# Performance work log

Measured on AMD Instinct MI355X. Metric: run time of the kernel, lower is better.

The kernel has to match this reference:

```python
import jax, jax.numpy as jnp
import numpy as np

B = 256        # number of graphs (mol rows)
N = 262144     # total residues
H = 128        # hidden_dim


def setup_inputs() -> dict:
    key = jax.random.key(0)
    ks = jax.random.split(key, 8)
    mol = jax.random.normal(ks[0], (B, H), dtype=jnp.float32)
    prot = jax.random.normal(ks[1], (N, H), dtype=jnp.float32)
    batch = jnp.sort(jax.random.randint(ks[2], (N,), 0, B)).astype(jnp.int64)
    s = 1.0 / np.sqrt(H)
    Wq = jax.random.uniform(ks[3], (H, H), jnp.float32, -s, s)
    bq = jax.random.uniform(ks[4], (H,), jnp.float32, -s, s)
    Wk = jax.random.uniform(ks[5], (H, H), jnp.float32, -s, s)
    bk = jax.random.uniform(ks[6], (H,), jnp.float32, -s, s)
    sm = 1.0 / np.sqrt(2 * H)
    Wm = jax.random.uniform(ks[7], (1, 2 * H), jnp.float32, -sm, sm)  # merge, no bias
    return {"mol": mol, "prot": prot, "batch": batch,
            "Wq": Wq, "bq": bq, "Wk": Wk, "bk": bk, "Wm": Wm}


def reference(mol, prot, batch, Wq, bq, Wk, bk, Wm):
    q = jax.nn.relu(mol @ Wq.T + bq)                      # [B, H]
    # repeat_interleave(q, degree(batch)) with sorted batch == gather q[batch]
    r = q[batch]                                          # [N, H]
    k = jax.nn.relu(prot @ Wk.T + bk)                     # [N, H]
    score = jnp.concatenate([k, r], axis=-1) @ Wm.T       # [N, 1]
    # segment softmax over residues of each graph (stable)
    m = jax.ops.segment_max(score, batch, num_segments=B)  # [B, 1]
    e = jnp.exp(score - m[batch])                          # [N, 1]
    denom = jax.ops.segment_sum(e, batch, num_segments=B)  # [B, 1]
    attn = e / denom[batch]                                # [N, 1]
    o = jax.ops.segment_sum(k * attn, batch, num_segments=B)  # [B, H]
    return (o, q)
```

## Files before the change

kernel.cpp:

```cpp
#include <hip/hip_runtime.h>
#include <hip/hip_bf16.h>

#define H      128
#define NB     256
#define NRES   262144
#define CHUNK  128
#define NCHUNK (NRES / CHUNK)
#define PIECES 64
#define REC    136

typedef __attribute__((ext_vector_type(4))) float f32x4;
typedef __attribute__((ext_vector_type(8))) short short8;

__device__ __forceinline__ short bf16cvt(float f) {
  unsigned u = __builtin_bit_cast(unsigned, f);
  unsigned r = (u + 0x7fffu + ((u >> 16) & 1u)) >> 16;
  return (short)r;
}

__device__ __forceinline__ float bf16tof(unsigned short u) {
  unsigned v = ((unsigned)u) << 16;
  return __builtin_bit_cast(float, v);
}

__device__ __forceinline__ short8 pack_bf16x8(f32x4 x, f32x4 y) {
  short8 v;
  v[0] = bf16cvt(x[0]); v[1] = bf16cvt(x[1]);
  v[2] = bf16cvt(x[2]); v[3] = bf16cvt(x[3]);
  v[4] = bf16cvt(y[0]); v[5] = bf16cvt(y[1]);
  v[6] = bf16cvt(y[2]); v[7] = bf16cvt(y[3]);
  return v;
}

__device__ __forceinline__ int lower_bound_i(const int* __restrict__ a, int n, int v) {
  int lo = 0, hi = n;
  while (lo < hi) { int mid = (lo + hi) >> 1; if (a[mid] < v) lo = mid + 1; else hi = mid; }
  return lo;
}

__global__ __launch_bounds__(256) void prep(
    const float* __restrict__ mol, const float* __restrict__ Wq,
    const float* __restrict__ bq, const float* __restrict__ Wk,
    float* __restrict__ out, short* __restrict__ wkp) {
  int bid = blockIdx.x, tid = threadIdx.x;
  if (bid < NB) {
    if (tid < H) {
      const float* mrow = mol + bid * H;
      const float* wrow = Wq + tid * H;
      float acc = bq[tid];
#pragma unroll 8
      for (int j = 0; j < H; ++j) acc = fmaf(mrow[j], wrow[j], acc);
      out[NB * H + bid * H + tid] = fmaxf(acc, 0.f);
    }
  } else {
    int slot = (bid - NB) * 256 + tid;
    int f = slot >> 6, l = slot & 63;
    int ct = f >> 2, kk = f & 3;
    const float* src = Wk + (ct * 16 + (l & 15)) * H + kk * 32 + (l >> 4) * 8;
    f32x4 x = *(const f32x4*)src;
    f32x4 y = *(const f32x4*)(src + 4);
    *(short8*)&wkp[slot * 8] = pack_bf16x8(x, y);
  }
}

__global__ __launch_bounds__(256) void chunkkern(
    const float* __restrict__ prot, const int* __restrict__ batch,
    const short* __restrict__ wkp, const float* __restrict__ bk,
    const float* __restrict__ Wm, float* __restrict__ part) {
  __shared__ short bfrag[2048 * 8];
  __shared__ unsigned short k_sh[CHUNK * 132];
  __shared__ float score_sh[CHUNK];
  __shared__ float e_sh[CHUNK];
  __shared__ float vhalf[H];
  __shared__ int   batch_sh[CHUNK];
  __shared__ float red[4], red2[4];

  int tid = threadIdx.x;
  int c0row = blockIdx.x * CHUNK;

  for (int i = tid; i < 2048; i += 256)
    *(short8*)&bfrag[i * 8] = *(const short8*)&wkp[i * 8];
  if (tid < CHUNK) batch_sh[tid] = batch[c0row + tid];
  __syncthreads();

  int w = tid >> 6, l = tid & 63;
  int cg = l & 15, kg = l >> 4;
  float wm1v[8], bkv[8];
#pragma unroll
  for (int ct = 0; ct < 8; ++ct) { wm1v[ct] = Wm[ct * 16 + cg]; bkv[ct] = bk[ct * 16 + cg]; }

#pragma unroll
  for (int tile = 0; tile < 2; ++tile) {
    int rbase = w * 32 + tile * 16;
    const float* pbase = prot + (c0row + rbase + cg) * H + kg * 8;
    short8 a[4];
#pragma unroll
    for (int kk = 0; kk < 4; ++kk) {
      f32x4 x = *(const f32x4*)(pbase + kk * 32);
      f32x4 y = *(const f32x4*)(pbase + kk * 32 + 4);
      a[kk] = pack_bf16x8(x, y);
    }
    f32x4 acc[8];
#pragma unroll
    for (int ct = 0; ct < 8; ++ct) acc[ct] = (f32x4){0.f, 0.f, 0.f, 0.f};
#pragma unroll
    for (int ct = 0; ct < 8; ++ct)
#pragma unroll
      for (int kk = 0; kk < 4; ++kk) {
        short8 bf = *(const short8*)&bfrag[((ct * 4 + kk) * 64 + l) * 8];
        acc[ct] = __builtin_amdgcn_mfma_f32_16x16x32_bf16(a[kk], bf, acc[ct], 0, 0, 0);
      }
    float p0 = 0.f, p1 = 0.f, p2 = 0.f, p3 = 0.f;
    int row0 = rbase + kg * 4;
#pragma unroll
    for (int ct = 0; ct < 8; ++ct) {
      float v0 = fmaxf(acc[ct][0] + bkv[ct], 0.f);
      float v1 = fmaxf(acc[ct][1] + bkv[ct], 0.f);
      float v2 = fmaxf(acc[ct][2] + bkv[ct], 0.f);
      float v3 = fmaxf(acc[ct][3] + bkv[ct], 0.f);
      p0 += v0 * wm1v[ct]; p1 += v1 * wm1v[ct];
      p2 += v2 * wm1v[ct]; p3 += v3 * wm1v[ct];
      int colb = ct * 16 + cg;
      k_sh[(row0 + 0) * 132 + colb] = (unsigned short)bf16cvt(v0);
      k_sh[(row0 + 1) * 132 + colb] = (unsigned short)bf16cvt(v1);
      k_sh[(row0 + 2) * 132 + colb] = (unsigned short)bf16cvt(v2);
      k_sh[(row0 + 3) * 132 + colb] = (unsigned short)bf16cvt(v3);
    }
#pragma unroll
    for (int off = 1; off < 16; off <<= 1) {
      p0 += __shfl_xor(p0, off); p1 += __shfl_xor(p1, off);
      p2 += __shfl_xor(p2, off); p3 += __shfl_xor(p3, off);
    }
    if (cg < 4) {
      int j = l & 3;
      float pv = (j == 0) ? p0 : (j == 1) ? p1 : (j == 2) ? p2 : p3;
      score_sh[rbase + kg * 4 + j] = pv;
    }
  }
  __syncthreads();

  int b0 = batch_sh[0], b1 = batch_sh[CHUNK - 1];
  int slot = blockIdx.x & (PIECES - 1);
  for (int b = b0; b <= b1; ++b) {
    int lo, hi;
    { int L = 0, R = CHUNK; while (L < R) { int M = (L + R) >> 1; if (batch_sh[M] < b) L = M + 1; else R = M; } lo = L; }
    { int L = 0, R = CHUNK; while (L < R) { int M = (L + R) >> 1; if (batch_sh[M] <= b) L = M + 1; else R = M; } hi = L; }
    if (hi > lo) {
      float x = (tid < CHUNK && tid >= lo && tid < hi) ? score_sh[tid] : -3.0e38f;
#pragma unroll
      for (int off = 32; off >= 1; off >>= 1) x = fmaxf(x, __shfl_xor(x, off));
      if (l == 0) red[w] = x;
      __syncthreads();
      float m_loc = fmaxf(fmaxf(red[0], red[1]), fmaxf(red[2], red[3]));
      float e = 0.f;
      if (tid < CHUNK && tid >= lo && tid < hi) { e = __expf(score_sh[tid] - m_loc); e_sh[tid] = e; }
      float s = e;
#pragma unroll
      for (int off = 32; off >= 1; off >>= 1) s += __shfl_xor(s, off);
      if (l == 0) red2[w] = s;
      __syncthreads();
      float s_loc = red2[0] + red2[1] + red2[2] + red2[3];
      int c = tid & 127, half = tid >> 7;
      float acc = 0.f;
      for (int r = lo + half; r < hi; r += 2)
        acc += e_sh[r] * bf16tof(k_sh[r * 132 + c]);
      if (half) vhalf[c] = acc;
      __syncthreads();
      float* pp = part + ((size_t)b * PIECES + slot) * REC;
      if (!half) pp[8 + c] = acc + vhalf[c];
      if (tid == 0) { pp[0] = m_loc; pp[1] = s_loc; }
      __syncthreads();
    }
  }
}

__global__ __launch_bounds__(128) void combine(
    const int* __restrict__ batch, const float* __restrict__ part,
    float* __restrict__ out) {
  int b = blockIdx.x, c = threadIdx.x;
  int start = lower_bound_i(batch, NRES, b);
  int end = lower_bound_i(batch, NRES, b + 1);
  if (end <= start) { out[b * H + c] = 0.f; return; }
  int c0 = start >> 7, c1 = (end - 1) >> 7;
  float m = -3.0e38f;
  for (int ch = c0; ch <= c1; ++ch)
    m = fmaxf(m, part[((size_t)b * PIECES + (ch & (PIECES - 1))) * REC]);
  float denom = 0.f, v = 0.f;
  for (int ch = c0; ch <= c1; ++ch) {
    const float* pp = part + ((size_t)b * PIECES + (ch & (PIECES - 1))) * REC;
    float wgt = __expf(pp[0] - m);
    denom += pp[1] * wgt;
    v += pp[8 + c] * wgt;
  }
  out[b * H + c] = (denom > 0.f) ? v / denom : 0.f;
}

extern "C" void kernel_launch(void* const* d_in, const int* in_sizes, int n_in,
                              void* d_out, int out_size, void* d_ws, size_t ws_size,
                              hipStream_t stream) {
  const float* mol   = (const float*)d_in[0];
  const float* prot  = (const float*)d_in[1];
  const int*   batch = (const int*)d_in[2];
  const float* Wq    = (const float*)d_in[3];
  const float* bq    = (const float*)d_in[4];
  const float* Wk    = (const float*)d_in[5];
  const float* bk    = (const float*)d_in[6];
  const float* Wm    = (const float*)d_in[7];
  float* out = (float*)d_out;

  short* wkp  = (short*)d_ws;
  float* part = (float*)((char*)d_ws + 32768);

  hipLaunchKernelGGL(prep, dim3(NB + 8), dim3(256), 0, stream, mol, Wq, bq, Wk, out, wkp);
  hipLaunchKernelGGL(chunkkern, dim3(NCHUNK), dim3(256), 0, stream, prot, batch, wkp, bk, Wm, part);
  hipLaunchKernelGGL(combine, dim3(NB), dim3(128), 0, stream, batch, part, out);
}
```

Measured before the change: 242.8 us.

## Fuse prep into main kernel and keep per-wave softmax partials in registers

Merges the prep kernel into the chunk kernel. Each block now converts Wk to bf16 fragments itself, and extra blocks compute the q projection. The segment softmax and weighted sum are done per wave over 32-row windows straight from the MFMA accumulator registers, which removes the LDS staging of k, the block-wide barriers and the binary searches. The cost is redundant Wk conversion in every block, four times as many partial records, and more combine work per graph.

```diff
diff --git a/kernel.cpp b/kernel.cpp
--- a/kernel.cpp
+++ b/kernel.cpp
@@ -6,7 +6,8 @@
 #define NRES   262144
 #define CHUNK  128
 #define NCHUNK (NRES / CHUNK)
-#define PIECES 64
+#define QBLK   (NB / 2)
+#define PIECES 128
 #define REC    136
 
 typedef __attribute__((ext_vector_type(4))) float f32x4;
@@ -16,11 +17,6 @@
   unsigned u = __builtin_bit_cast(unsigned, f);
   unsigned r = (u + 0x7fffu + ((u >> 16) & 1u)) >> 16;
   return (short)r;
-}
-
-__device__ __forceinline__ float bf16tof(unsigned short u) {
-  unsigned v = ((unsigned)u) << 16;
-  return __builtin_bit_cast(float, v);
 }
 
 __device__ __forceinline__ short8 pack_bf16x8(f32x4 x, f32x4 y) {
@@ -38,49 +34,41 @@
   return lo;
 }
 
-__global__ __launch_bounds__(256) void prep(
-    const float* __restrict__ mol, const float* __restrict__ Wq,
-    const float* __restrict__ bq, const float* __restrict__ Wk,
-    float* __restrict__ out, short* __restrict__ wkp) {
-  int bid = blockIdx.x, tid = threadIdx.x;
-  if (bid < NB) {
-    if (tid < H) {
-      const float* mrow = mol + bid * H;
-      const float* wrow = Wq + tid * H;
-      float acc = bq[tid];
+__global__ __launch_bounds__(256) void flashkern(
+    const float* __restrict__ prot, const int* __restrict__ batch,
+    const float* __restrict__ Wk, const float* __restrict__ bk,
+    const float* __restrict__ Wm, const float* __restrict__ mol,
+    const float* __restrict__ Wq, const float* __restrict__ bq,
+    float* __restrict__ out, float* __restrict__ part) {
+  int tid = threadIdx.x;
+
+  if (blockIdx.x >= NCHUNK) {
+    int b = (blockIdx.x - NCHUNK) * 2 + (tid >> 7);
+    int h = tid & 127;
+    const float* mrow = mol + b * H;
+    const float* wrow = Wq + h * H;
+    float acc = bq[h];
 #pragma unroll 8
-      for (int j = 0; j < H; ++j) acc = fmaf(mrow[j], wrow[j], acc);
-      out[NB * H + bid * H + tid] = fmaxf(acc, 0.f);
-    }
-  } else {
-    int slot = (bid - NB) * 256 + tid;
+    for (int j = 0; j < H; ++j) acc = fmaf(mrow[j], wrow[j], acc);
+    out[NB * H + b * H + h] = fmaxf(acc, 0.f);
+    return;
+  }
+
+  __shared__ short bfrag[2048 * 8];
+  __shared__ float score_sh[CHUNK];
+  __shared__ int   batch_sh[CHUNK];
+
+  int c0row = blockIdx.x * CHUNK;
+
+  for (int slot = tid; slot < 2048; slot += 256) {
     int f = slot >> 6, l = slot & 63;
     int ct = f >> 2, kk = f & 3;
     const float* src = Wk + (ct * 16 + (l & 15)) * H + kk * 32 + (l >> 4) * 8;
     f32x4 x = *(const f32x4*)src;
     f32x4 y = *(const f32x4*)(src + 4);
-    *(short8*)&wkp[slot * 8] = pack_bf16x8(x, y);
-  }
-}
-
-__global__ __launch_bounds__(256) void chunkkern(
-    const float* __restrict__ prot, const int* __restrict__ batch,
-    const short* __restrict__ wkp, const float* __restrict__ bk,
-    const float* __restrict__ Wm, float* __restrict__ part) {
-  __shared__ short bfrag[2048 * 8];
-  __shared__ unsigned short k_sh[CHUNK * 132];
-  __shared__ float score_sh[CHUNK];
-  __shared__ float e_sh[CHUNK];
-  __shared__ float vhalf[H];
-  __shared__ int   batch_sh[CHUNK];
-  __shared__ float red[4], red2[4];
-
-  int tid = threadIdx.x;
-  int c0row = blockIdx.x * CHUNK;
-
-  for (int i = tid; i < 2048; i += 256)
-    *(short8*)&bfrag[i * 8] = *(const short8*)&wkp[i * 8];
-  if (tid < CHUNK) batch_sh[tid] = batch[c0row + tid];
+    *(short8*)&bfrag[slot * 8] = pack_bf16x8(x, y);
+  }
+  if (tid < 32) ((int4*)batch_sh)[tid] = ((const int4*)(batch + c0row))[tid];
   __syncthreads();
 
   int w = tid >> 6, l = tid & 63;
@@ -89,10 +77,12 @@
 #pragma unroll
   for (int ct = 0; ct < 8; ++ct) { wm1v[ct] = Wm[ct * 16 + cg]; bkv[ct] = bk[ct * 16 + cg]; }
 
+  f32x4 acc0[8], acc1[8];
 #pragma unroll
   for (int tile = 0; tile < 2; ++tile) {
+    f32x4* acc = tile ? acc1 : acc0;
     int rbase = w * 32 + tile * 16;
-    const float* pbase = prot + (c0row + rbase + cg) * H + kg * 8;
+    const float* pbase = prot + (size_t)(c0row + rbase + cg) * H + kg * 8;
     short8 a[4];
 #pragma unroll
     for (int kk = 0; kk < 4; ++kk) {
@@ -100,7 +90,6 @@
       f32x4 y = *(const f32x4*)(pbase + kk * 32 + 4);
       a[kk] = pack_bf16x8(x, y);
     }
-    f32x4 acc[8];
 #pragma unroll
     for (int ct = 0; ct < 8; ++ct) acc[ct] = (f32x4){0.f, 0.f, 0.f, 0.f};
 #pragma unroll
@@ -111,20 +100,14 @@
         acc[ct] = __builtin_amdgcn_mfma_f32_16x16x32_bf16(a[kk], bf, acc[ct], 0, 0, 0);
       }
     float p0 = 0.f, p1 = 0.f, p2 = 0.f, p3 = 0.f;
-    int row0 = rbase + kg * 4;
 #pragma unroll
     for (int ct = 0; ct < 8; ++ct) {
-      float v0 = fmaxf(acc[ct][0] + bkv[ct], 0.f);
-      float v1 = fmaxf(acc[ct][1] + bkv[ct], 0.f);
-      float v2 = fmaxf(acc[ct][2] + bkv[ct], 0.f);
-      float v3 = fmaxf(acc[ct][3] + bkv[ct], 0.f);
-      p0 += v0 * wm1v[ct]; p1 += v1 * wm1v[ct];
-      p2 += v2 * wm1v[ct]; p3 += v3 * wm1v[ct];
-      int colb = ct * 16 + cg;
-      k_sh[(row0 + 0) * 132 + colb] = (unsigned short)bf16cvt(v0);
-      k_sh[(row0 + 1) * 132 + colb] = (unsigned short)bf16cvt(v1);
-      k_sh[(row0 + 2) * 132 + colb] = (unsigned short)bf16cvt(v2);
-      k_sh[(row0 + 3) * 132 + colb] = (unsigned short)bf16cvt(v3);
+      acc[ct][0] = fmaxf(acc[ct][0] + bkv[ct], 0.f);
+      acc[ct][1] = fmaxf(acc[ct][1] + bkv[ct], 0.f);
+      acc[ct][2] = fmaxf(acc[ct][2] + bkv[ct], 0.f);
+      acc[ct][3] = fmaxf(acc[ct][3] + bkv[ct], 0.f);
+      p0 += acc[ct][0] * wm1v[ct]; p1 += acc[ct][1] * wm1v[ct];
+      p2 += acc[ct][2] * wm1v[ct]; p3 += acc[ct][3] * wm1v[ct];
     }
 #pragma unroll
     for (int off = 1; off < 16; off <<= 1) {
@@ -139,38 +122,48 @@
   }
   __syncthreads();
 
-  int b0 = batch_sh[0], b1 = batch_sh[CHUNK - 1];
-  int slot = blockIdx.x & (PIECES - 1);
-  for (int b = b0; b <= b1; ++b) {
-    int lo, hi;
-    { int L = 0, R = CHUNK; while (L < R) { int M = (L + R) >> 1; if (batch_sh[M] < b) L = M + 1; else R = M; } lo = L; }
-    { int L = 0, R = CHUNK; while (L < R) { int M = (L + R) >> 1; if (batch_sh[M] <= b) L = M + 1; else R = M; } hi = L; }
-    if (hi > lo) {
-      float x = (tid < CHUNK && tid >= lo && tid < hi) ? score_sh[tid] : -3.0e38f;
-#pragma unroll
-      for (int off = 32; off >= 1; off >>= 1) x = fmaxf(x, __shfl_xor(x, off));
-      if (l == 0) red[w] = x;
-      __syncthreads();
-      float m_loc = fmaxf(fmaxf(red[0], red[1]), fmaxf(red[2], red[3]));
-      float e = 0.f;
-      if (tid < CHUNK && tid >= lo && tid < hi) { e = __expf(score_sh[tid] - m_loc); e_sh[tid] = e; }
-      float s = e;
-#pragma unroll
-      for (int off = 32; off >= 1; off >>= 1) s += __shfl_xor(s, off);
-      if (l == 0) red2[w] = s;
-      __syncthreads();
-      float s_loc = red2[0] + red2[1] + red2[2] + red2[3];
-      int c = tid & 127, half = tid >> 7;
-      float acc = 0.f;
-      for (int r = lo + half; r < hi; r += 2)
-        acc += e_sh[r] * bf16tof(k_sh[r * 132 + c]);
-      if (half) vhalf[c] = acc;
-      __syncthreads();
-      float* pp = part + ((size_t)b * PIECES + slot) * REC;
-      if (!half) pp[8 + c] = acc + vhalf[c];
-      if (tid == 0) { pp[0] = m_loc; pp[1] = s_loc; }
-      __syncthreads();
-    }
+  float sc[8]; int bt[8];
+#pragma unroll
+  for (int i = 0; i < 8; ++i) {
+    int rl = w * 32 + (i >> 2) * 16 + kg * 4 + (i & 3);
+    sc[i] = score_sh[rl];
+    bt[i] = batch_sh[rl];
+  }
+  float myscore = (l < 32) ? score_sh[w * 32 + l] : -3.0e38f;
+  int   myb     = (l < 32) ? batch_sh[w * 32 + l] : -1;
+  int bfirst = batch_sh[w * 32], blast = batch_sh[w * 32 + 31];
+  int win = blockIdx.x * 4 + w;
+  int slot = win & (PIECES - 1);
+
+  for (int b = bfirst; b <= blast; ++b) {
+    float x = (myb == b) ? myscore : -3.0e38f;
+#pragma unroll
+    for (int off = 32; off >= 1; off >>= 1) x = fmaxf(x, __shfl_xor(x, off));
+    float m = x;
+    float e = (myb == b) ? __expf(myscore - m) : 0.f;
+#pragma unroll
+    for (int off = 32; off >= 1; off >>= 1) e += __shfl_xor(e, off);
+    float s = e;
+    float op[8] = {0.f, 0.f, 0.f, 0.f, 0.f, 0.f, 0.f, 0.f};
+#pragma unroll
+    for (int i = 0; i < 8; ++i) {
+      float ei = (bt[i] == b) ? __expf(sc[i] - m) : 0.f;
+      const f32x4* acc = (i < 4) ? acc0 : acc1;
+      int j = i & 3;
+#pragma unroll
+      for (int ct = 0; ct < 8; ++ct) op[ct] = fmaf(ei, acc[ct][j], op[ct]);
+    }
+#pragma unroll
+    for (int ct = 0; ct < 8; ++ct) {
+      op[ct] += __shfl_xor(op[ct], 16);
+      op[ct] += __shfl_xor(op[ct], 32);
+    }
+    float* pp = part + ((size_t)b * PIECES + slot) * REC;
+    if (l < 16) {
+#pragma unroll
+      for (int ct = 0; ct < 8; ++ct) pp[8 + ct * 16 + l] = op[ct];
+    }
+    if (l == 0) { pp[0] = m; pp[1] = s; }
   }
 }
 
@@ -181,7 +174,7 @@
   int start = lower_bound_i(batch, NRES, b);
   int end = lower_bound_i(batch, NRES, b + 1);
   if (end <= start) { out[b * H + c] = 0.f; return; }
-  int c0 = start >> 7, c1 = (end - 1) >> 7;
+  int c0 = start >> 5, c1 = (end - 1) >> 5;
   float m = -3.0e38f;
   for (int ch = c0; ch <= c1; ++ch)
     m = fmaxf(m, part[((size_t)b * PIECES + (ch & (PIECES - 1))) * REC]);
@@ -190,7 +183,7 @@
     const float* pp = part + ((size_t)b * PIECES + (ch & (PIECES - 1))) * REC;
     float wgt = __expf(pp[0] - m);
     denom += pp[1] * wgt;
-    v += pp[8 + c] * wgt;
+    v = fmaf(pp[8 + c], wgt, v);
   }
   out[b * H + c] = (denom > 0.f) ? v / denom : 0.f;
 }
@@ -208,10 +201,9 @@
   const float* Wm    = (const float*)d_in[7];
   float* out = (float*)d_out;
 
-  short* wkp  = (short*)d_ws;
-  float* part = (float*)((char*)d_ws + 32768);
-
-  hipLaunchKernelGGL(prep, dim3(NB + 8), dim3(256), 0, stream, mol, Wq, bq, Wk, out, wkp);
-  hipLaunchKernelGGL(chunkkern, dim3(NCHUNK), dim3(256), 0, stream, prot, batch, wkp, bk, Wm, part);
+  float* part = (float*)d_ws;
+
+  hipLaunchKernelGGL(flashkern, dim3(NCHUNK + QBLK), dim3(256), 0, stream,
+                     prot, batch, Wk, bk, Wm, mol, Wq, bq, out, part);
   hipLaunchKernelGGL(combine, dim3(NB), dim3(128), 0, stream, batch, part, out);
 }
```

New measurement: 245.2 us. Within noise of the previous version (+1.0%).
